# Kernel optimization log

Measured on AMD Instinct MI355X. Metric: run time of the kernel, lower is better.

Reference implementation:

```python
import jax, jax.numpy as jnp
import numpy as np

B, K, SZ, D = 256, 16, 512, 8

def setup_inputs() -> dict:
    key = jax.random.key(0)
    k1, k2 = jax.random.split(key)
    x = jax.random.normal(k1, (B, SZ, D), dtype=jnp.float32)
    cluster_centers = jax.random.normal(k2, (K, SZ, D), dtype=jnp.float32)
    return {"x": x, "cluster_centers": cluster_centers}

def _dists(x, centers):
    # x: [B, sz, d]; centers: [K, sz, d]
    b, sz, d = x.shape
    k = centers.shape[0]
    # fft_sz = 2 ** int(log2(2*sz - 1) + 1)  (matches n_bits computation in normalized_cc)
    fft_sz = 2 ** int(np.log2(2 * sz - 1) + 1)
    # The module's hand-rolled dft matrix is cos(-2pi kn/N) + i sin(-2pi kn/N),
    # i.e. exactly the standard DFT of the zero-padded signal -> use jnp.fft.
    Fx = jnp.fft.fft(x, n=fft_sz, axis=1)            # [B, F, d]
    Fc = jnp.fft.fft(centers, n=fft_sz, axis=1)      # [K, F, d]
    # cc(s1, s2) = real(ifft(F1 * conj(F2))), batched over all (i, j) pairs
    prod = Fx[:, None, :, :] * jnp.conj(Fc)[None, :, :, :]   # [B, K, F, d]
    cc = jnp.real(jnp.fft.ifft(prod, axis=2))                # [B, K, F, d]
    # cc_ = cat(cc[-(sz-1):], cc[:sz])  -> length 2*sz - 1 along lag axis
    cc_cat = jnp.concatenate([cc[:, :, -(sz - 1):, :], cc[:, :, :sz, :]], axis=2)
    # norms: norm1 = Frobenius norm per sample; norm2 = arange(K) (as in forward)
    norms1 = jnp.linalg.norm(x.reshape(b, -1), axis=1)       # [B]
    norms2 = jnp.arange(k, dtype=x.dtype)                    # [K]
    denom = norms1[:, None] * norms2[None, :]                # [B, K]
    denom = jnp.where(denom < 1e-9, jnp.inf, denom)
    ncc = cc_cat.sum(axis=-1) / denom[:, :, None]            # [B, K, 2sz-1]
    return ncc.max(axis=2)                                   # [B, K]

def reference(x, cluster_centers):
    dists = _dists(x, cluster_centers)
    labels = jnp.argmin(1.0 - dists, axis=1)
    return (labels, dists)
```

## Files before the change

kernel.cpp:

```cpp
#include <hip/hip_runtime.h>
#include <math.h>


#define NB 256
#define NK 16
#define NS 512
#define ND 8

typedef int intx4 __attribute__((ext_vector_type(4)));

#define MFMA_I8(a, b, c) __builtin_amdgcn_mfma_i32_16x16x64_i8(a, b, c, 0, 0, 0)

__device__ __forceinline__ int q8(float v, float s) {
    return (int)rintf(fminf(fmaxf(v * s, -127.f), 127.f));
}
__device__ __forceinline__ unsigned pk4(int a, int b, int c, int d) {
    return (a & 255) | ((b & 255) << 8) | ((c & 255) << 16) | ((unsigned)(d & 255) << 24);
}

__global__ __launch_bounds__(1024, 4) void kshape_kernel(
    const float* __restrict__ x, const float* __restrict__ c, float* __restrict__ out)
{
    __shared__ __align__(16) char xqE[560 * 16];
    __shared__ __align__(16) char xqO[560 * 16];
    __shared__ __align__(16) char Bq[68 * 64 * 16];
    __shared__ float Mc[16];
    __shared__ float redn[16], redm[16];
    __shared__ float s_Mb, s_nrm;
    __shared__ int   wredi[16][16];
    __shared__ float dd[16];

    const int tid = threadIdx.x;
    const int b   = blockIdx.x;
    const int L   = tid & 63;
    const int wu  = __builtin_amdgcn_readfirstlane(tid >> 6);

    {
        int4 z = {0, 0, 0, 0};
        if (tid < 560) { ((int4*)xqE)[tid] = z; ((int4*)xqO)[tid] = z; }
        if (tid < 256) ((int4*)(Bq + 64 * 64 * 16))[tid] = z;
    }

    const float4* x4 = (const float4*)(x + (size_t)b * (NS * ND));
    float4 v = x4[tid];
    float am = fmaxf(fmaxf(fabsf(v.x), fabsf(v.y)), fmaxf(fabsf(v.z), fabsf(v.w)));
    float ss = v.x * v.x + v.y * v.y + v.z * v.z + v.w * v.w;
    const float4* cw = (const float4*)(c + (size_t)wu * (NS * ND));
    float cm = 0.f;
    #pragma unroll
    for (int i = 0; i < 16; ++i) {
        float4 w = cw[L + 64 * i];
        cm = fmaxf(cm, fmaxf(fmaxf(fabsf(w.x), fabsf(w.y)), fmaxf(fabsf(w.z), fabsf(w.w))));
    }
    #pragma unroll
    for (int off = 32; off; off >>= 1) {
        ss += __shfl_down(ss, off);
        am = fmaxf(am, __shfl_down(am, off));
        cm = fmaxf(cm, __shfl_down(cm, off));
    }
    if (L == 0) { redn[wu] = ss; redm[wu] = am; Mc[wu] = cm; }
    __syncthreads();

    float Mb = redm[0];
    #pragma unroll
    for (int i = 1; i < 16; ++i) Mb = fmaxf(Mb, redm[i]);
    if (tid == 0) {
        float t = 0.f;
        #pragma unroll
        for (int i = 0; i < 16; ++i) t += redn[i];
        s_nrm = sqrtf(t);
        s_Mb  = Mb;
    }

    const float sx = (Mb > 0.f) ? 127.f / Mb : 0.f;
    if (tid < 512) {
        int row = 511 + tid;
        float4 a = x4[2 * tid], bb = x4[2 * tid + 1];
        unsigned lo = pk4(q8(a.x, sx), q8(a.y, sx), q8(a.z, sx), q8(a.w, sx));
        unsigned hi = pk4(q8(bb.x, sx), q8(bb.y, sx), q8(bb.z, sx), q8(bb.w, sx));
        uint2 pr = make_uint2(lo, hi);
        *(uint2*)(xqE + (row >> 1) * 16 + (row & 1) * 8) = pr;
        int lineO = (row & 1) ? (row >> 1) : (row >> 1) - 1;
        int offO  = (row & 1) ? 0 : 8;
        *(uint2*)(xqO + lineO * 16 + offO) = pr;
    }

    #pragma unroll
    for (int i = 0; i < 4; ++i) {
        int f = tid + 1024 * i;
        int kc = f >> 6, Lf = f & 63, n = Lf & 15, qd = Lf >> 4;
        int t0 = 8 * kc + 2 * qd;
        const float4* cn = (const float4*)(c + (size_t)n * (NS * ND));
        float4 a = cn[2 * t0], b2 = cn[2 * t0 + 1], c2 = cn[2 * t0 + 2], d2 = cn[2 * t0 + 3];
        float sc = (Mc[n] > 0.f) ? 127.f / Mc[n] : 0.f;
        int4 w;
        w.x = pk4(q8(a.x, sc), q8(a.y, sc), q8(a.z, sc), q8(a.w, sc));
        w.y = pk4(q8(b2.x, sc), q8(b2.y, sc), q8(b2.z, sc), q8(b2.w, sc));
        w.z = pk4(q8(c2.x, sc), q8(c2.y, sc), q8(c2.z, sc), q8(c2.w, sc));
        w.w = pk4(q8(d2.x, sc), q8(d2.y, sc), q8(d2.z, sc), q8(d2.w, sc));
        ((int4*)Bq)[f] = w;
    }
    __syncthreads();

    const int m    = L & 15;
    const int quad = L >> 4;
    const int a0  = 56 - 8 * wu;
    const int klo = (a0 > 0) ? a0 : 0;
    const int kh_ = 127 - 8 * wu;
    const int khi = (kh_ > 63) ? 63 : kh_;

    const char* base = ((m & 1) == 0) ? xqE : xqO;
    const char* ga   = base + ((((64 * wu + m) - (m & 1)) >> 1) + quad) * 16;
    const char* Bl = Bq + L * 16;

    intx4 Q[8];
    #pragma unroll
    for (int i = 0; i < 8; ++i) Q[i] = *(const intx4*)(ga + 64 * (klo + i));
    intx4 Bv[4];
    #pragma unroll
    for (int i = 0; i < 4; ++i) Bv[i] = *(const intx4*)(Bl + (size_t)(klo + i) * 1024);

    intx4 acc[4] = {};

    for (int kc0 = klo; kc0 <= khi; kc0 += 8) {
        #pragma unroll
        for (int s = 0; s < 8; ++s) {
            const int kc = kc0 + s;
            intx4 bcur = Bv[s & 3];
            acc[0] = MFMA_I8(Q[(s + 0) & 7], bcur, acc[0]);
            acc[1] = MFMA_I8(Q[(s + 2) & 7], bcur, acc[1]);
            acc[2] = MFMA_I8(Q[(s + 4) & 7], bcur, acc[2]);
            acc[3] = MFMA_I8(Q[(s + 6) & 7], bcur, acc[3]);
            Q[s & 7]  = *(const intx4*)(ga + 64 * (kc + 8));
            Bv[s & 3] = *(const intx4*)(Bl + (size_t)(kc + 4) * 1024);
        }
    }

    int vmax = (int)0x80000000;
    #pragma unroll
    for (int r = 0; r < 4; ++r) {
        #pragma unroll
        for (int e = 0; e < 4; ++e) {
            bool phantom = (wu == 15) & (r == 3) & (quad == 3) & (e == 3);
            int val = phantom ? (int)0x80000000 : acc[r][e];
            vmax = (val > vmax) ? val : vmax;
        }
    }
    { int o = __shfl_xor(vmax, 16); vmax = (o > vmax) ? o : vmax; }
    { int o = __shfl_xor(vmax, 32); vmax = (o > vmax) ? o : vmax; }
    if (quad == 0) wredi[wu][m] = vmax;
    __syncthreads();

    if (tid < 16) {
        int mm = wredi[0][tid];
        #pragma unroll
        for (int i = 1; i < 16; ++i) mm = (wredi[i][tid] > mm) ? wredi[i][tid] : mm;
        float scale = s_Mb * Mc[tid] * (1.0f / 16129.0f);
        float denom = s_nrm * (float)tid;
        float d = (denom < 1e-9f) ? 0.f : ((float)mm * scale) / denom;
        dd[tid] = d;
        out[NB + b * NK + tid] = d;
    }
    __syncthreads();
    if (tid == 0) {
        float best = dd[0]; int lab = 0;
        #pragma unroll
        for (int k = 1; k < NK; ++k) if (dd[k] > best) { best = dd[k]; lab = k; }
        out[b] = (float)lab;
    }
}

extern "C" void kernel_launch(void* const* d_in, const int* in_sizes, int n_in,
                              void* d_out, int out_size, void* d_ws, size_t ws_size,
                              hipStream_t stream) {
    const float* x = (const float*)d_in[0];
    const float* c = (const float*)d_in[1];
    float* out = (float*)d_out;
    kshape_kernel<<<NB, 1024, 0, stream>>>(x, c, out);
}
```

Before: 70.63 us.

## Hoist cluster-center quantization into a separate pre-pass kernel

Adds a small pack_kernel that computes each center's max-abs scale and packs the int8-quantized centers into the MFMA B-layout once in workspace. The main kernel then copies the prepacked buffer into LDS instead of having all 256 blocks redundantly reduce and quantize all 16 centers. This removes repeated global reads of the full center tensor and the float-to-int8 work per block. In exchange it adds a second launch and a dependency between the two kernels.

```diff
diff --git a/kernel.cpp b/kernel.cpp
--- a/kernel.cpp
+++ b/kernel.cpp
@@ -18,15 +18,52 @@
     return (a & 255) | ((b & 255) << 8) | ((c & 255) << 16) | ((unsigned)(d & 255) << 24);
 }
 
+__global__ __launch_bounds__(256) void pack_kernel(
+    const float* __restrict__ c, char* __restrict__ Bq, float* __restrict__ Mc)
+{
+    const int tid = threadIdx.x;
+    const int blk = blockIdx.x;
+    if (blk == 16) {
+        int4 z = {0, 0, 0, 0};
+        ((int4*)(Bq + 64 * 1024))[tid] = z;
+        return;
+    }
+    __shared__ float red[4];
+    const int n = blk;
+    const float4* cn = (const float4*)(c + (size_t)n * (NS * ND));
+    float cm = 0.f;
+    #pragma unroll
+    for (int i = 0; i < 4; ++i) {
+        float4 v = cn[tid + 256 * i];
+        cm = fmaxf(cm, fmaxf(fmaxf(fabsf(v.x), fabsf(v.y)), fmaxf(fabsf(v.z), fabsf(v.w))));
+    }
+    #pragma unroll
+    for (int off = 32; off; off >>= 1) cm = fmaxf(cm, __shfl_down(cm, off));
+    if ((tid & 63) == 0) red[tid >> 6] = cm;
+    __syncthreads();
+    const float M = fmaxf(fmaxf(red[0], red[1]), fmaxf(red[2], red[3]));
+    if (tid == 0) Mc[n] = M;
+    const float sc = (M > 0.f) ? 127.f / M : 0.f;
+    const int kc = tid >> 2, qd = tid & 3;
+    const int f4 = 16 * kc + 4 * qd;
+    float4 a = cn[f4], b2 = cn[f4 + 1], c2 = cn[f4 + 2], d2 = cn[f4 + 3];
+    int4 w;
+    w.x = pk4(q8(a.x, sc),  q8(a.y, sc),  q8(a.z, sc),  q8(a.w, sc));
+    w.y = pk4(q8(b2.x, sc), q8(b2.y, sc), q8(b2.z, sc), q8(b2.w, sc));
+    w.z = pk4(q8(c2.x, sc), q8(c2.y, sc), q8(c2.z, sc), q8(c2.w, sc));
+    w.w = pk4(q8(d2.x, sc), q8(d2.y, sc), q8(d2.z, sc), q8(d2.w, sc));
+    *(int4*)(Bq + (size_t)kc * 1024 + (size_t)(qd * 16 + n) * 16) = w;
+}
+
 __global__ __launch_bounds__(1024, 4) void kshape_kernel(
-    const float* __restrict__ x, const float* __restrict__ c, float* __restrict__ out)
+    const float* __restrict__ x, const char* __restrict__ Bqg,
+    const float* __restrict__ Mc, float* __restrict__ out)
 {
     __shared__ __align__(16) char xqE[560 * 16];
     __shared__ __align__(16) char xqO[560 * 16];
     __shared__ __align__(16) char Bq[68 * 64 * 16];
-    __shared__ float Mc[16];
+    __shared__ float sMc[16];
     __shared__ float redn[16], redm[16];
-    __shared__ float s_Mb, s_nrm;
     __shared__ int   wredi[16][16];
     __shared__ float dd[16];
 
@@ -38,42 +75,33 @@
     {
         int4 z = {0, 0, 0, 0};
         if (tid < 560) { ((int4*)xqE)[tid] = z; ((int4*)xqO)[tid] = z; }
-        if (tid < 256) ((int4*)(Bq + 64 * 64 * 16))[tid] = z;
-    }
+    }
+    #pragma unroll
+    for (int i = 0; i < 5; ++i) {
+        int idx = tid + 1024 * i;
+        if (idx < 4352) ((int4*)Bq)[idx] = ((const int4*)Bqg)[idx];
+    }
+    if (tid < 16) sMc[tid] = Mc[tid];
 
     const float4* x4 = (const float4*)(x + (size_t)b * (NS * ND));
-    float4 v = x4[tid];
-    float am = fmaxf(fmaxf(fabsf(v.x), fabsf(v.y)), fmaxf(fabsf(v.z), fabsf(v.w)));
-    float ss = v.x * v.x + v.y * v.y + v.z * v.z + v.w * v.w;
-    const float4* cw = (const float4*)(c + (size_t)wu * (NS * ND));
-    float cm = 0.f;
-    #pragma unroll
-    for (int i = 0; i < 16; ++i) {
-        float4 w = cw[L + 64 * i];
-        cm = fmaxf(cm, fmaxf(fmaxf(fabsf(w.x), fabsf(w.y)), fmaxf(fabsf(w.z), fabsf(w.w))));
-    }
-    #pragma unroll
-    for (int off = 32; off; off >>= 1) {
-        ss += __shfl_down(ss, off);
-        am = fmaxf(am, __shfl_down(am, off));
-        cm = fmaxf(cm, __shfl_down(cm, off));
-    }
-    if (L == 0) { redn[wu] = ss; redm[wu] = am; Mc[wu] = cm; }
-    __syncthreads();
-
-    float Mb = redm[0];
-    #pragma unroll
-    for (int i = 1; i < 16; ++i) Mb = fmaxf(Mb, redm[i]);
-    if (tid == 0) {
-        float t = 0.f;
-        #pragma unroll
-        for (int i = 0; i < 16; ++i) t += redn[i];
-        s_nrm = sqrtf(t);
-        s_Mb  = Mb;
-    }
-
-    const float sx = (Mb > 0.f) ? 127.f / Mb : 0.f;
+    {
+        float4 v = x4[tid];
+        float am = fmaxf(fmaxf(fabsf(v.x), fabsf(v.y)), fmaxf(fabsf(v.z), fabsf(v.w)));
+        float ss = v.x * v.x + v.y * v.y + v.z * v.z + v.w * v.w;
+        #pragma unroll
+        for (int off = 32; off; off >>= 1) {
+            ss += __shfl_down(ss, off);
+            am = fmaxf(am, __shfl_down(am, off));
+        }
+        if (L == 0) { redn[wu] = ss; redm[wu] = am; }
+    }
+    __syncthreads();
+
     if (tid < 512) {
+        float Mb = redm[0];
+        #pragma unroll
+        for (int i = 1; i < 16; ++i) Mb = fmaxf(Mb, redm[i]);
+        const float sx = (Mb > 0.f) ? 127.f / Mb : 0.f;
         int row = 511 + tid;
         float4 a = x4[2 * tid], bb = x4[2 * tid + 1];
         unsigned lo = pk4(q8(a.x, sx), q8(a.y, sx), q8(a.z, sx), q8(a.w, sx));
@@ -83,22 +111,6 @@
         int lineO = (row & 1) ? (row >> 1) : (row >> 1) - 1;
         int offO  = (row & 1) ? 0 : 8;
         *(uint2*)(xqO + lineO * 16 + offO) = pr;
-    }
-
-    #pragma unroll
-    for (int i = 0; i < 4; ++i) {
-        int f = tid + 1024 * i;
-        int kc = f >> 6, Lf = f & 63, n = Lf & 15, qd = Lf >> 4;
-        int t0 = 8 * kc + 2 * qd;
-        const float4* cn = (const float4*)(c + (size_t)n * (NS * ND));
-        float4 a = cn[2 * t0], b2 = cn[2 * t0 + 1], c2 = cn[2 * t0 + 2], d2 = cn[2 * t0 + 3];
-        float sc = (Mc[n] > 0.f) ? 127.f / Mc[n] : 0.f;
-        int4 w;
-        w.x = pk4(q8(a.x, sc), q8(a.y, sc), q8(a.z, sc), q8(a.w, sc));
-        w.y = pk4(q8(b2.x, sc), q8(b2.y, sc), q8(b2.z, sc), q8(b2.w, sc));
-        w.z = pk4(q8(c2.x, sc), q8(c2.y, sc), q8(c2.z, sc), q8(c2.w, sc));
-        w.w = pk4(q8(d2.x, sc), q8(d2.y, sc), q8(d2.z, sc), q8(d2.w, sc));
-        ((int4*)Bq)[f] = w;
     }
     __syncthreads();
 
@@ -155,8 +167,13 @@
         int mm = wredi[0][tid];
         #pragma unroll
         for (int i = 1; i < 16; ++i) mm = (wredi[i][tid] > mm) ? wredi[i][tid] : mm;
-        float scale = s_Mb * Mc[tid] * (1.0f / 16129.0f);
-        float denom = s_nrm * (float)tid;
+        float Mb = redm[0];
+        float t = 0.f;
+        #pragma unroll
+        for (int i = 0; i < 16; ++i) { Mb = fmaxf(Mb, redm[i]); t += redn[i]; }
+        float nrm = sqrtf(t);
+        float scale = Mb * sMc[tid] * (1.0f / 16129.0f);
+        float denom = nrm * (float)tid;
         float d = (denom < 1e-9f) ? 0.f : ((float)mm * scale) / denom;
         dd[tid] = d;
         out[NB + b * NK + tid] = d;
@@ -176,5 +193,9 @@
     const float* x = (const float*)d_in[0];
     const float* c = (const float*)d_in[1];
     float* out = (float*)d_out;
-    kshape_kernel<<<NB, 1024, 0, stream>>>(x, c, out);
-}
+    char*  Bq  = (char*)d_ws;
+    float* Mc  = (float*)((char*)d_ws + 70656);
+
+    pack_kernel<<<17, 256, 0, stream>>>(c, Bq, Mc);
+    kshape_kernel<<<NB, 1024, 0, stream>>>(x, Bq, Mc, out);
+}
```

Measured after the change: 65.64 us. -7.1%, faster.
